# Kernel optimization log

Measured on AMD Instinct MI355X. Metric: run time of the kernel, lower is better.

## Reference

```python
import jax, jax.numpy as jnp
import numpy as np

N = 100000  # nodes per cluster
E = 1000000  # nonzeros per sparse Laplacian
D = 64       # embedding_size
LEAKY_SLOPE = 0.2  # tf.nn.leaky_relu default alpha


def spmm(rows, cols, vals, dense, num_rows):
    """Sparse [num_rows, M] (COO) @ dense [M, D] -> [num_rows, D]."""
    gathered = vals[:, None] * dense[cols]  # [E, D]
    return jax.ops.segment_sum(gathered, rows, num_segments=num_rows)


def setup_inputs() -> dict:
    key = jax.random.key(0)
    ks = jax.random.split(key, 10)
    return {
        "ebs": jax.random.normal(ks[0], (N, D), dtype=jnp.float32),
        "entity_ebs": jax.random.normal(ks[1], (N, D), dtype=jnp.float32),
        "W_side": jax.random.normal(ks[2], (D, D), dtype=jnp.float32),
        "W_dot": jax.random.normal(ks[3], (D, D), dtype=jnp.float32),
        "LI_vals": jax.random.uniform(ks[4], (E,), dtype=jnp.float32),
        "L_vals": jax.random.uniform(ks[5], (E,), dtype=jnp.float32),
        "LI_rows": jax.random.randint(ks[6], (E,), 0, N, dtype=jnp.int32),
        "LI_cols": jax.random.randint(ks[7], (E,), 0, N, dtype=jnp.int32),
        "L_rows": jax.random.randint(ks[8], (E,), 0, N, dtype=jnp.int32),
        "L_cols": jax.random.randint(ks[9], (E,), 0, N, dtype=jnp.int32),
    }


def reference(ebs, entity_ebs, W_side, W_dot, LI_vals, L_vals,
              LI_rows, LI_cols, L_rows, L_cols) -> jnp.ndarray:
    # __build_weight_graph
    LI_side_embed = spmm(LI_rows, LI_cols, LI_vals, ebs, N)   # [N, D]
    L_side_embed = spmm(L_rows, L_cols, L_vals, ebs, N)       # [N, D]
    sum_embed = LI_side_embed @ W_side                          # [N, D]
    dot_embed = (L_side_embed * entity_ebs) @ W_dot             # [N, D]
    return jax.nn.leaky_relu(sum_embed + dot_embed, negative_slope=LEAKY_SLOPE)
```

## Files before the change

### kernel.cpp

```cpp
#include <hip/hip_runtime.h>

#define D        64
#define BINROWS  64
#define SUBCAP   256
#define NSHARD   8
#define NBINS_MAX 1568
#define CHUNK    3072
#define PER_TH   (CHUNK / 256)
#define FS16     72
#define CURSTRIDE 16
#define FTH      512

typedef __attribute__((ext_vector_type(8))) short short8;
typedef __attribute__((ext_vector_type(4))) float floatx4;

__device__ __forceinline__ unsigned short f2bf(float f) {
    unsigned u = __float_as_uint(f);
    u += 0x7fffu + ((u >> 16) & 1u);
    return (unsigned short)(u >> 16);
}
__device__ __forceinline__ float bf2f(unsigned short u) {
    return __uint_as_float(((unsigned)u) << 16);
}

__global__ __launch_bounds__(256) void expand_bin_kernel(
    const int* __restrict__ LI_rows, const int* __restrict__ LI_cols, const float* __restrict__ LI_vals,
    const int* __restrict__ L_rows,  const int* __restrict__ L_cols,  const float* __restrict__ L_vals,
    int* __restrict__ cursorP, uint2* __restrict__ seg, int E, int nbins,
    const float* __restrict__ ebs, unsigned short* __restrict__ ebs16, int total4,
    const float* __restrict__ W_side, const float* __restrict__ W_dot,
    unsigned short* __restrict__ Wfrag)
{
    __shared__ uint2 sorted[CHUNK];
    __shared__ unsigned short sbin[CHUNK];
    __shared__ int hist[NBINS_MAX];
    __shared__ int cur[NBINS_MAX];
    __shared__ int gbase[NBINS_MAX];
    __shared__ int tsum[256];

    int t  = threadIdx.x;

    for (int i = blockIdx.x * 256 + t; i < total4; i += gridDim.x * 256) {
        float4 v = ((const float4*)ebs)[i];
        ushort4 o;
        o.x = f2bf(v.x); o.y = f2bf(v.y); o.z = f2bf(v.z); o.w = f2bf(v.w);
        ((ushort4*)ebs16)[i] = o;
    }
    if (blockIdx.x < 4) {
        int tt = blockIdx.x * 256 + t;
        int f = tt >> 6;
        int l = tt & 63;
        int jt = f >> 2, kt = f & 3;
        int q = l >> 4, nl = l & 15;
        int nn = jt * 16 + nl;
#pragma unroll
        for (int j = 0; j < 8; ++j) {
            int k = kt * 32 + q * 8 + j;
            float w = (k < 64) ? W_side[k * 64 + nn] : W_dot[(k - 64) * 64 + nn];
            Wfrag[(size_t)f * 512 + l * 8 + j] = f2bf(w);
        }
    }

    int c0 = blockIdx.x * CHUNK;
    int sh = blockIdx.x & (NSHARD - 1);
    int twoE = 2 * E;
    int chunkcnt = twoE - c0; if (chunkcnt > CHUNK) chunkcnt = CHUNK;

    for (int b = t; b < NBINS_MAX; b += 256) hist[b] = 0;
    __syncthreads();

    unsigned rm[PER_TH];
    uint2    cv[PER_TH];

#pragma unroll
    for (int k = 0; k < PER_TH; ++k) {
        int e = c0 + k * 256 + t;
        rm[k] = 0xFFFFFFFFu;
        if (e < twoE) {
            int m = (e >= E) ? 1 : 0;
            int r, cl; float v;
            if (m) { r = L_rows[e - E]; cl = L_cols[e - E]; v = L_vals[e - E]; }
            else   { r = LI_rows[e];    cl = LI_cols[e];    v = LI_vals[e]; }
            rm[k] = (unsigned)r | ((unsigned)m << 17);
            cv[k] = make_uint2((unsigned)cl, __float_as_uint(v));
            atomicAdd(&hist[r >> 6], 1);
        }
    }
    __syncthreads();

    int loc[7]; int tot = 0;
    if (t < 224) {
#pragma unroll
        for (int i = 0; i < 7; ++i) { loc[i] = tot; tot += hist[t * 7 + i]; }
    }
    tsum[t] = (t < 224) ? tot : 0;
    __syncthreads();
    for (int step = 1; step < 256; step <<= 1) {
        int add = (t >= step) ? tsum[t - step] : 0;
        __syncthreads();
        tsum[t] += add;
        __syncthreads();
    }
    int tbase = tsum[t] - ((t < 224) ? tot : 0);
    if (t < 224) {
#pragma unroll
        for (int i = 0; i < 7; ++i) {
            int key = t * 7 + i;
            cur[key] = tbase + loc[i];
        }
    }
    __syncthreads();

    for (int b = t; b < nbins; b += 256) {
        int c = hist[b];
        gbase[b] = c ? atomicAdd(&cursorP[(sh * NBINS_MAX + b) * CURSTRIDE], c) : 0;
    }

#pragma unroll
    for (int k = 0; k < PER_TH; ++k) {
        unsigned g = rm[k];
        if (g == 0xFFFFFFFFu) continue;
        int r   = (int)(g & 0x1FFFFu);
        int m   = (int)((g >> 17) & 1u);
        int bin = r >> 6;
        int rank = atomicAdd(&cur[bin], 1);
        sorted[rank] = make_uint2(((unsigned)m << 23) | ((unsigned)(r & 63) << 17) | cv[k].x, cv[k].y);
        sbin[rank]   = (unsigned short)bin;
    }
    __syncthreads();

    for (int i = t; i < chunkcnt; i += 256) {
        int bin = sbin[i];
        int off = cur[bin] - hist[bin];
        int pos = gbase[bin] + (i - off);
        if (pos < SUBCAP)
            seg[((size_t)(sh * NBINS_MAX) + bin) * SUBCAP + pos] = sorted[i];
    }
}

__global__ __launch_bounds__(FTH) void fused_kernel(
    const uint2* __restrict__ seg, const int* __restrict__ cursorP,
    const unsigned short* __restrict__ ebs16,
    const float* __restrict__ entity,
    const unsigned short* __restrict__ Wfrag,
    float* __restrict__ out, int n)
{
    __shared__ __align__(16) char shmem[2 * BINROWS * FS16 * 2];
    __shared__ int hist[128];
    __shared__ int offs[128];
    __shared__ int cur[128];
    uint2* sseg = (uint2*)shmem;
    unsigned short* facc = (unsigned short*)shmem;

    int t = threadIdx.x;
    int b = blockIdx.x;

    if (t < 128) hist[t] = 0;
    __syncthreads();

    int clen[NSHARD];
#pragma unroll
    for (int sh = 0; sh < NSHARD; ++sh) {
        int c = cursorP[(sh * NBINS_MAX + b) * CURSTRIDE];
        clen[sh] = c < SUBCAP ? c : SUBCAP;
    }
    uint2 held[4];
    unsigned hmask = 0;
#pragma unroll
    for (int k = 0; k < 4; ++k) {
        int i   = k * FTH + t;
        int sh  = i >> 8;
        int pos = i & 255;
        if (pos < clen[sh]) {
            held[k] = seg[((size_t)(sh * NBINS_MAX) + b) * SUBCAP + pos];
            hmask |= (1u << k);
            atomicAdd(&hist[(held[k].x >> 17) & 127u], 1);
        }
    }
    __syncthreads();

    if (t < 128) offs[t] = hist[t];
    __syncthreads();
    for (int step = 1; step < 128; step <<= 1) {
        int add = 0;
        if (t < 128 && t >= step) add = offs[t - step];
        __syncthreads();
        if (t < 128) offs[t] += add;
        __syncthreads();
    }
    if (t < 128) {
        int excl = offs[t] - hist[t];
        offs[t] = excl;
        cur[t]  = excl;
    }
    __syncthreads();

#pragma unroll
    for (int k = 0; k < 4; ++k) {
        if (hmask & (1u << k)) {
            unsigned key = (held[k].x >> 17) & 127u;
            int rank = atomicAdd(&cur[key], 1);
            sseg[rank] = held[k];
        }
    }
    __syncthreads();

    int g  = t >> 4;
    int l4 = (t & 15) << 2;
    int beg[4], len[4], lenm1[4];
    int maxlen = 0;
#pragma unroll
    for (int kk = 0; kk < 4; ++kk) {
        int key = g * 4 + kk;
        beg[kk]   = offs[key];
        len[kk]   = hist[key];
        lenm1[kk] = len[kk] > 0 ? len[kk] - 1 : 0;
        maxlen = max(maxlen, len[kk]);
    }
    floatx4 a4[4];
#pragma unroll
    for (int kk = 0; kk < 4; ++kk) a4[kk] = (floatx4){0.f, 0.f, 0.f, 0.f};

    for (int s = 0; s < maxlen; s += 2) {
        uint2 enA[4], enB[4];
#pragma unroll
        for (int kk = 0; kk < 4; ++kk) {
            enA[kk] = sseg[beg[kk] + min(s,     lenm1[kk])];
            enB[kk] = sseg[beg[kk] + min(s + 1, lenm1[kk])];
        }
        __builtin_amdgcn_sched_barrier(0);
        ushort4 xA[4], xB[4];
#pragma unroll
        for (int kk = 0; kk < 4; ++kk) {
            unsigned ea = (s < len[kk]) ? (enA[kk].x & 0x1FFFFu) : 0u;
            xA[kk] = *(const ushort4*)(ebs16 + (ea << 6) + l4);
        }
#pragma unroll
        for (int kk = 0; kk < 4; ++kk) {
            unsigned eb = (s + 1 < len[kk]) ? (enB[kk].x & 0x1FFFFu) : 0u;
            xB[kk] = *(const ushort4*)(ebs16 + (eb << 6) + l4);
        }
        __builtin_amdgcn_sched_barrier(0);
#pragma unroll
        for (int kk = 0; kk < 4; ++kk) {
            float vv = (s < len[kk]) ? __uint_as_float(enA[kk].y) : 0.f;
            ushort4 x = xA[kk];
            a4[kk][0] += vv * bf2f(x.x);
            a4[kk][1] += vv * bf2f(x.y);
            a4[kk][2] += vv * bf2f(x.z);
            a4[kk][3] += vv * bf2f(x.w);
        }
#pragma unroll
        for (int kk = 0; kk < 4; ++kk) {
            float vv = (s + 1 < len[kk]) ? __uint_as_float(enB[kk].y) : 0.f;
            ushort4 x = xB[kk];
            a4[kk][0] += vv * bf2f(x.x);
            a4[kk][1] += vv * bf2f(x.y);
            a4[kk][2] += vv * bf2f(x.z);
            a4[kk][3] += vv * bf2f(x.w);
        }
    }
    __syncthreads();

#pragma unroll
    for (int kk = 0; kk < 4; ++kk) {
        int key = g * 4 + kk;
        ushort4 o;
        o.x = f2bf(a4[kk][0]); o.y = f2bf(a4[kk][1]);
        o.z = f2bf(a4[kk][2]); o.w = f2bf(a4[kk][3]);
        *(ushort4*)(facc + ((size_t)(key >> 6) * BINROWS + (key & 63)) * FS16 + l4) = o;
    }
    __syncthreads();

    if (t < 256) {
        int w = t >> 6;
        int l = t & 63;
        int q = l >> 4, mcol = l & 15;
        int rowbase = b * BINROWS + w * 16;
        int growA = rowbase + mcol;
        int binrow = w * 16 + mcol;
        const unsigned short* faccLI = facc;
        const unsigned short* faccL  = facc + BINROWS * FS16;

        floatx4 accv[4];
#pragma unroll
        for (int jt = 0; jt < 4; ++jt) accv[jt] = (floatx4){0.f, 0.f, 0.f, 0.f};

#pragma unroll
        for (int kt = 0; kt < 4; ++kt) {
            short8 af;
            if (kt < 2) {
                af = *(const short8*)(faccLI + (size_t)binrow * FS16 + kt * 32 + q * 8);
            } else {
                short8 lv = *(const short8*)(faccL + (size_t)binrow * FS16 + (kt - 2) * 32 + q * 8);
                float4 e0 = make_float4(0.f, 0.f, 0.f, 0.f), e1 = e0;
                if (growA < n) {
                    const float4* ep = (const float4*)(entity + (size_t)growA * D + (kt - 2) * 32 + q * 8);
                    e0 = ep[0]; e1 = ep[1];
                }
                af[0] = (short)f2bf(bf2f((unsigned short)lv[0]) * e0.x);
                af[1] = (short)f2bf(bf2f((unsigned short)lv[1]) * e0.y);
                af[2] = (short)f2bf(bf2f((unsigned short)lv[2]) * e0.z);
                af[3] = (short)f2bf(bf2f((unsigned short)lv[3]) * e0.w);
                af[4] = (short)f2bf(bf2f((unsigned short)lv[4]) * e1.x);
                af[5] = (short)f2bf(bf2f((unsigned short)lv[5]) * e1.y);
                af[6] = (short)f2bf(bf2f((unsigned short)lv[6]) * e1.z);
                af[7] = (short)f2bf(bf2f((unsigned short)lv[7]) * e1.w);
            }
#pragma unroll
            for (int jt = 0; jt < 4; ++jt) {
                const short8 bf = *(const short8*)(Wfrag + (size_t)(jt * 4 + kt) * 512 + (size_t)l * 8);
                accv[jt] = __builtin_amdgcn_mfma_f32_16x16x32_bf16(af, bf, accv[jt], 0, 0, 0);
            }
        }

#pragma unroll
        for (int jt = 0; jt < 4; ++jt) {
#pragma unroll
            for (int r = 0; r < 4; ++r) {
                int grow = rowbase + q * 4 + r;
                if (grow < n) {
                    float v = accv[jt][r];
                    v = v > 0.f ? v : 0.2f * v;
                    out[(size_t)grow * D + jt * 16 + mcol] = v;
                }
            }
        }
    }
}

__global__ void scatter_kernel(
    const float* __restrict__ LI_vals, const int* __restrict__ LI_rows, const int* __restrict__ LI_cols,
    const float* __restrict__ L_vals,  const int* __restrict__ L_rows,  const int* __restrict__ L_cols,
    const float* __restrict__ ebs,
    float* __restrict__ accLI, float* __restrict__ accL, int E)
{
    long long t = (long long)blockIdx.x * blockDim.x + threadIdx.x;
    long long e2 = t >> 4;
    if (e2 >= 2LL * E) return;
    int c = ((int)t & 15) << 2;
    const float* vals; const int* rows; const int* cols; float* acc; int e;
    if (e2 < E) { vals = LI_vals; rows = LI_rows; cols = LI_cols; acc = accLI; e = (int)e2; }
    else        { vals = L_vals;  rows = L_rows;  cols = L_cols;  acc = accL;  e = (int)(e2 - E); }
    float v = vals[e]; int r = rows[e]; int cl = cols[e];
    const float4 x = *(const float4*)(ebs + (size_t)cl * D + c);
    float* o = acc + (size_t)r * D + c;
    unsafeAtomicAdd(o + 0, v * x.x);
    unsafeAtomicAdd(o + 1, v * x.y);
    unsafeAtomicAdd(o + 2, v * x.z);
    unsafeAtomicAdd(o + 3, v * x.w);
}

__global__ __launch_bounds__(256) void epilogue_kernel(
    const float* __restrict__ acc, const float* __restrict__ entity,
    const float* __restrict__ W_side, const float* __restrict__ W_dot,
    float* __restrict__ out, int n)
{
    int lane = threadIdx.x & 63;
    int wave = (blockIdx.x << 2) | (threadIdx.x >> 6);
    int row  = (wave << 6) + lane;
    bool valid = row < n;
    const float* accLI = acc;
    const float* accL  = acc + (size_t)n * D;
    float a[D], b[D];
    if (valid) {
        const float4* ap = (const float4*)(accLI  + (size_t)row * D);
        const float4* lp = (const float4*)(accL   + (size_t)row * D);
        const float4* ep = (const float4*)(entity + (size_t)row * D);
#pragma unroll
        for (int qq = 0; qq < 16; ++qq) {
            float4 av = ap[qq]; float4 lv = lp[qq]; float4 ev = ep[qq];
            a[4*qq+0] = av.x; a[4*qq+1] = av.y; a[4*qq+2] = av.z; a[4*qq+3] = av.w;
            b[4*qq+0] = lv.x * ev.x; b[4*qq+1] = lv.y * ev.y;
            b[4*qq+2] = lv.z * ev.z; b[4*qq+3] = lv.w * ev.w;
        }
    } else {
#pragma unroll
        for (int qq = 0; qq < D; ++qq) { a[qq] = 0.f; b[qq] = 0.f; }
    }
    float4* op = (float4*)(out + (size_t)row * D);
#pragma unroll 1
    for (int jc = 0; jc < 16; ++jc) {
        float a0 = 0.f, a1 = 0.f, a2 = 0.f, a3 = 0.f;
#pragma unroll
        for (int k = 0; k < D; ++k) {
            float4 w1 = *(const float4*)(W_side + (k << 6) + (jc << 2));
            float4 w2 = *(const float4*)(W_dot  + (k << 6) + (jc << 2));
            a0 += a[k] * w1.x + b[k] * w2.x;
            a1 += a[k] * w1.y + b[k] * w2.y;
            a2 += a[k] * w1.z + b[k] * w2.z;
            a3 += a[k] * w1.w + b[k] * w2.w;
        }
        float4 r;
        r.x = a0 > 0.f ? a0 : 0.2f * a0;
        r.y = a1 > 0.f ? a1 : 0.2f * a1;
        r.z = a2 > 0.f ? a2 : 0.2f * a2;
        r.w = a3 > 0.f ? a3 : 0.2f * a3;
        if (valid) op[jc] = r;
    }
}

extern "C" void kernel_launch(void* const* d_in, const int* in_sizes, int n_in,
                              void* d_out, int out_size, void* d_ws, size_t ws_size,
                              hipStream_t stream) {
    const float* ebs     = (const float*)d_in[0];
    const float* entity  = (const float*)d_in[1];
    const float* W_side  = (const float*)d_in[2];
    const float* W_dot   = (const float*)d_in[3];
    const float* LI_vals = (const float*)d_in[4];
    const float* L_vals  = (const float*)d_in[5];
    const int*   LI_rows = (const int*)d_in[6];
    const int*   LI_cols = (const int*)d_in[7];
    const int*   L_rows  = (const int*)d_in[8];
    const int*   L_cols  = (const int*)d_in[9];
    float* out = (float*)d_out;

    int E = in_sizes[4];
    int n = in_sizes[0] / D;
    int nbins = (n + BINROWS - 1) / BINROWS;

    size_t curBytes = (size_t)NSHARD * NBINS_MAX * CURSTRIDE * sizeof(int);
    size_t segBytes = (size_t)NSHARD * NBINS_MAX * SUBCAP * sizeof(uint2);
    size_t ebsBytes = (size_t)n * D * sizeof(unsigned short);
    size_t wfBytes  = (size_t)16 * 512 * sizeof(unsigned short);
    size_t need = curBytes + segBytes + ebsBytes + wfBytes;

    if (ws_size >= need && nbins <= NBINS_MAX && n <= 131072) {
        int*            cursorP = (int*)d_ws;
        uint2*          seg     = (uint2*)((char*)d_ws + curBytes);
        unsigned short* ebs16   = (unsigned short*)((char*)d_ws + curBytes + segBytes);
        unsigned short* Wfrag   = (unsigned short*)((char*)d_ws + curBytes + segBytes + ebsBytes);

        hipMemsetAsync(cursorP, 0, curBytes, stream);

        int total4 = n * D / 4;
        int xblocks = (2 * E + CHUNK - 1) / CHUNK;
        expand_bin_kernel<<<xblocks, 256, 0, stream>>>(
            LI_rows, LI_cols, LI_vals, L_rows, L_cols, L_vals,
            cursorP, seg, E, nbins,
            ebs, ebs16, total4, W_side, W_dot, Wfrag);

        fused_kernel<<<nbins, FTH, 0, stream>>>(
            seg, cursorP, ebs16, entity, Wfrag, out, n);
    } else {
        size_t accBytes = (size_t)2 * n * D * sizeof(float);
        float* acc   = (float*)d_ws;
        float* accLI = acc;
        float* accL  = accLI + (size_t)n * D;
        hipMemsetAsync(d_ws, 0, accBytes, stream);
        long long totalThreads = 2LL * E * 16;
        int sblocks = (int)((totalThreads + 255) / 256);
        scatter_kernel<<<sblocks, 256, 0, stream>>>(
            LI_vals, LI_rows, LI_cols, L_vals, L_rows, L_cols, ebs, accLI, accL, E);
        int nTiles = (n + 63) / 64;
        epilogue_kernel<<<(nTiles + 3) / 4, 256, 0, stream>>>(
            acc, entity, W_side, W_dot, out, n);
    }
}
```

Baseline: 222.3 us.

## Reuse histogram atomic ranks and use wave-shuffle scan in binning kernel

The histogram atomicAdd now returns each element's rank within its bin, so the second pass of shared-memory atomics during scatter is gone. The block-wide Hillis-Steele scan with many barriers is replaced by a wavefront shuffle scan plus a small cross-wave sum. The global cursor atomics are folded into the per-thread prefix loop. CHUNK shrinks from 3072 to 2560 to make room for the extra per-thread rank registers, which means more blocks and more global cursor atomics.

```diff
diff --git a/kernel.cpp b/kernel.cpp
--- a/kernel.cpp
+++ b/kernel.cpp
@@ -5,7 +5,7 @@
 #define SUBCAP   256
 #define NSHARD   8
 #define NBINS_MAX 1568
-#define CHUNK    3072
+#define CHUNK    2560
 #define PER_TH   (CHUNK / 256)
 #define FS16     72
 #define CURSTRIDE 16
@@ -33,10 +33,9 @@
 {
     __shared__ uint2 sorted[CHUNK];
     __shared__ unsigned short sbin[CHUNK];
-    __shared__ int hist[NBINS_MAX];
     __shared__ int cur[NBINS_MAX];
     __shared__ int gbase[NBINS_MAX];
-    __shared__ int tsum[256];
+    __shared__ int wsum[4];
 
     int t  = threadIdx.x;
 
@@ -66,11 +65,12 @@
     int twoE = 2 * E;
     int chunkcnt = twoE - c0; if (chunkcnt > CHUNK) chunkcnt = CHUNK;
 
-    for (int b = t; b < NBINS_MAX; b += 256) hist[b] = 0;
+    for (int b = t; b < NBINS_MAX; b += 256) cur[b] = 0;
     __syncthreads();
 
     unsigned rm[PER_TH];
     uint2    cv[PER_TH];
+    int      rank[PER_TH];
 
 #pragma unroll
     for (int k = 0; k < PER_TH; ++k) {
@@ -83,7 +83,7 @@
             else   { r = LI_rows[e];    cl = LI_cols[e];    v = LI_vals[e]; }
             rm[k] = (unsigned)r | ((unsigned)m << 17);
             cv[k] = make_uint2((unsigned)cl, __float_as_uint(v));
-            atomicAdd(&hist[r >> 6], 1);
+            rank[k] = atomicAdd(&cur[r >> 6], 1);
         }
     }
     __syncthreads();
@@ -91,50 +91,52 @@
     int loc[7]; int tot = 0;
     if (t < 224) {
 #pragma unroll
-        for (int i = 0; i < 7; ++i) { loc[i] = tot; tot += hist[t * 7 + i]; }
-    }
-    tsum[t] = (t < 224) ? tot : 0;
-    __syncthreads();
-    for (int step = 1; step < 256; step <<= 1) {
-        int add = (t >= step) ? tsum[t - step] : 0;
-        __syncthreads();
-        tsum[t] += add;
-        __syncthreads();
-    }
-    int tbase = tsum[t] - ((t < 224) ? tot : 0);
+        for (int i = 0; i < 7; ++i) { loc[i] = cur[t * 7 + i]; tot += loc[i]; }
+    }
+    int lane = t & 63, wv = t >> 6;
+    int inc = tot;
+#pragma unroll
+    for (int off = 1; off < 64; off <<= 1) {
+        int y = __shfl_up(inc, off, 64);
+        if (lane >= off) inc += y;
+    }
+    if (lane == 63) wsum[wv] = inc;
+    __syncthreads();
+    int pre = 0;
+#pragma unroll
+    for (int w = 0; w < 4; ++w) pre += (w < wv) ? wsum[w] : 0;
+    int tbase = pre + inc - tot;
     if (t < 224) {
+        int run = tbase;
 #pragma unroll
         for (int i = 0; i < 7; ++i) {
             int key = t * 7 + i;
-            cur[key] = tbase + loc[i];
-        }
-    }
-    __syncthreads();
-
-    for (int b = t; b < nbins; b += 256) {
-        int c = hist[b];
-        gbase[b] = c ? atomicAdd(&cursorP[(sh * NBINS_MAX + b) * CURSTRIDE], c) : 0;
-    }
+            int c = loc[i];
+            cur[key] = run;
+            gbase[key] = c ? atomicAdd(&cursorP[(sh * NBINS_MAX + key) * CURSTRIDE], c) : 0;
+            run += c;
+        }
+    }
+    __syncthreads();
 
 #pragma unroll
     for (int k = 0; k < PER_TH; ++k) {
-        unsigned g = rm[k];
-        if (g == 0xFFFFFFFFu) continue;
-        int r   = (int)(g & 0x1FFFFu);
-        int m   = (int)((g >> 17) & 1u);
+        unsigned gg = rm[k];
+        if (gg == 0xFFFFFFFFu) continue;
+        int r   = (int)(gg & 0x1FFFFu);
+        int m   = (int)((gg >> 17) & 1u);
         int bin = r >> 6;
-        int rank = atomicAdd(&cur[bin], 1);
-        sorted[rank] = make_uint2(((unsigned)m << 23) | ((unsigned)(r & 63) << 17) | cv[k].x, cv[k].y);
-        sbin[rank]   = (unsigned short)bin;
+        int pos = cur[bin] + rank[k];
+        sorted[pos] = make_uint2(((unsigned)m << 23) | ((unsigned)(r & 63) << 17) | cv[k].x, cv[k].y);
+        sbin[pos]   = (unsigned short)bin;
     }
     __syncthreads();
 
     for (int i = t; i < chunkcnt; i += 256) {
         int bin = sbin[i];
-        int off = cur[bin] - hist[bin];
-        int pos = gbase[bin] + (i - off);
-        if (pos < SUBCAP)
-            seg[((size_t)(sh * NBINS_MAX) + bin) * SUBCAP + pos] = sorted[i];
+        int gpos = gbase[bin] + (i - cur[bin]);
+        if (gpos < SUBCAP)
+            seg[((size_t)(sh * NBINS_MAX) + bin) * SUBCAP + gpos] = sorted[i];
     }
 }
 
```

New measurement: 223.3 us (median of 2 runs). Within noise of the previous version (+0.5%).
